# Optimization experiments

Hardware: AMD Instinct MI355X
Metric: run time of the kernel (lower is better)

The kernel has to match this reference:

```python
import jax, jax.numpy as jnp
import numpy as np

B, D, G, L = 8, 128, 2048, 24
GF = G // 2 + 1  # rfft bins
EPS = 1e-5


def setup_inputs() -> dict:
    key = jax.random.key(0)
    ks = jax.random.split(key, 6)
    x = jax.random.normal(ks[0], (B, D, G), dtype=jnp.float32)
    Phi_f = jax.random.normal(ks[1], (L, GF), dtype=jnp.float32) * 0.1
    Theta = jax.random.normal(ks[2], (L, D, D), dtype=jnp.float32) * (1.0 / np.sqrt(D))
    ln_gamma = jnp.ones((D,), dtype=jnp.float32)
    ln_beta = jnp.zeros((D,), dtype=jnp.float32)
    fc1_w = jax.random.normal(ks[3], (2 * D, D), dtype=jnp.float32) * (1.0 / np.sqrt(D))
    fc1_b = jnp.zeros((2 * D,), dtype=jnp.float32)
    fc2_w = jax.random.normal(ks[4], (D, 2 * D), dtype=jnp.float32) * (1.0 / np.sqrt(2 * D))
    fc2_b = jnp.zeros((D,), dtype=jnp.float32)
    return {
        'x': x, 'Phi_f': Phi_f, 'Theta': Theta,
        'ln_gamma': ln_gamma, 'ln_beta': ln_beta,
        'fc1_w': fc1_w, 'fc1_b': fc1_b, 'fc2_w': fc2_w, 'fc2_b': fc2_b,
    }


def reference(x, Phi_f, Theta, ln_gamma, ln_beta, fc1_w, fc1_b, fc2_w, fc2_b):
    # x: (B, D, G). LayerNorm over the lifting (channel) dim D.
    mean = jnp.mean(x, axis=1, keepdims=True)
    var = jnp.var(x, axis=1, keepdims=True)
    z = (x - mean) * jax.lax.rsqrt(var + EPS)
    z = z * ln_gamma[None, :, None] + ln_beta[None, :, None]

    # Spectral convolution with each Hilbert filter.
    Xf = jnp.fft.rfft(z, axis=-1)                       # (B, D, GF) complex
    Uf = Xf[:, :, None, :] * jnp.conj(Phi_f)[None, None]  # (B, D, L, GF)
    U = jnp.fft.irfft(Uf, n=G, axis=-1)                 # (B, D, L, G)

    # Per-filter channel mixing then reduction over filters:
    # einsum('bdln,lhd->bhln') followed by sum over l, fused:
    S = jnp.einsum('bdlg,lhd->bhg', U, Theta)           # (B, D, G)

    # Pointwise MLP (Conv1d kernel_size=1 == channel matmul).
    H = jnp.einsum('hd,bdg->bhg', fc1_w, S) + fc1_b[None, :, None]
    H = jax.nn.gelu(H, approximate=False)
    out = jnp.einsum('dh,bhg->bdg', fc2_w, H) + fc2_b[None, :, None]
    return x + out
```

## Files before the change

### kernel.cpp

```cpp
#include <hip/hip_runtime.h>
#include <math.h>


#define B_   8
#define D_   128
#define G_   2048
#define L_   24
#define GF_  1025
#define BD_  1024
#define C2_  2050
#define CP_  2080
#define MW_  2176
#define KP2_ 2112
#define DD_  16384

#define PB_GWI0 2176
#define PB_LN0  4224
#define PB_CV0  4288
#define PB_TT0  4354
#define PB_END  4610

typedef __attribute__((ext_vector_type(8))) short  short8v;
typedef __attribute__((ext_vector_type(4))) float  float4v;

union FU { float f; unsigned int u; };
union V8 { short8v v; ushort u[8]; };
union V4 { uint2 p; ushort u[4]; };

static __device__ __forceinline__ float bf2f(ushort h) {
    FU v; v.u = ((unsigned int)h) << 16; return v.f;
}
static __device__ __forceinline__ ushort f2bf(float f) {
    FU v; v.f = f;
    unsigned int r = v.u + 0x7fffu + ((v.u >> 16) & 1u);
    return (ushort)(r >> 16);
}
static __device__ __forceinline__ void async16(const void* g, void* l) {
    __builtin_amdgcn_global_load_lds(
        (const __attribute__((address_space(1))) void*)g,
        (__attribute__((address_space(3))) void*)l, 16, 0, 0);
}
static __device__ __forceinline__ int is_f32(const unsigned int* graw) {
    return graw[0] == 0x3F800000u;
}

__global__ __launch_bounds__(256) void k_pre(
        const void* __restrict__ x_raw,  const void* __restrict__ th_raw,
        const unsigned int* __restrict__ graw, const void* __restrict__ be_raw,
        const void* __restrict__ w1_raw, const void* __restrict__ b1_raw,
        const void* __restrict__ w2_raw, const void* __restrict__ b2_raw,
        ushort* __restrict__ z,  ushort* __restrict__ wf,
        ushort* __restrict__ wi, ushort* __restrict__ thT,
        ushort* __restrict__ w1c, ushort* __restrict__ b1c,
        ushort* __restrict__ w2c, ushort* __restrict__ b2c) {
    __shared__ ushort T[L_][72];
    int bid = blockIdx.x, tid = threadIdx.x;

    if (bid < PB_GWI0) {
        int c  = bid;
        int g0 = tid * 8;
        V8 v;
        if (c >= C2_) {
            #pragma unroll
            for (int j = 0; j < 8; ++j) v.u[j] = 0;
        } else {
            int f = c >> 1, im = c & 1;
            #pragma unroll
            for (int j = 0; j < 8; ++j) {
                int g = g0 + j;
                int r = (f * g) & (G_ - 1);
                float th = (float)r * (6.283185307179586f / (float)G_);
                v.u[j] = f2bf(im ? -__sinf(th) : __cosf(th));
            }
        }
        *(short8v*)(wf + (size_t)c * G_ + g0) = v.v;
    } else if (bid < PB_LN0) {
        int g = bid - PB_GWI0;
        for (int ch = tid; ch < KP2_ / 8; ch += 256) {
            int c0 = ch * 8;
            V8 v;
            #pragma unroll
            for (int j = 0; j < 8; ++j) {
                int c = c0 + j;
                if (c >= C2_) { v.u[j] = 0; continue; }
                int f = c >> 1, im = c & 1;
                float a = (f == 0 || f == G_ / 2) ? (1.f / G_) : (2.f / G_);
                int r = (f * g) & (G_ - 1);
                float th = (float)r * (6.283185307179586f / (float)G_);
                v.u[j] = f2bf(im ? -a * __sinf(th) : a * __cosf(th));
            }
            *(short8v*)(wi + (size_t)g * KP2_ + c0) = v.v;
        }
    } else if (bid < PB_CV0) {
        int fl = is_f32(graw);
        int lb = bid - PB_LN0;
        int b  = lb >> 3;
        int g  = (lb & 7) * 256 + tid;
        float s = 0.f, ss = 0.f;
        if (fl) {
            const float* xp = (const float*)x_raw + (size_t)b * D_ * G_ + g;
            for (int d = 0; d < D_; ++d) {
                float v = xp[(size_t)d * G_];
                s += v; ss += v * v;
            }
        } else {
            const ushort* xp = (const ushort*)x_raw + (size_t)b * D_ * G_ + g;
            for (int d = 0; d < D_; ++d) {
                float v = bf2f(xp[(size_t)d * G_]);
                s += v; ss += v * v;
            }
        }
        float mean = s * (1.f / D_);
        float var  = ss * (1.f / D_) - mean * mean;
        float inv  = rsqrtf(var + 1e-5f);
        ushort* zp = z + (size_t)b * D_ * G_ + g;
        if (fl) {
            const float* xp = (const float*)x_raw + (size_t)b * D_ * G_ + g;
            const float* gp = (const float*)graw;
            const float* bp = (const float*)be_raw;
            for (int d = 0; d < D_; ++d) {
                float o = (xp[(size_t)d * G_] - mean) * inv * gp[d] + bp[d];
                zp[(size_t)d * G_] = f2bf(o);
            }
        } else {
            const ushort* xp = (const ushort*)x_raw + (size_t)b * D_ * G_ + g;
            const ushort* gp = (const ushort*)graw;
            const ushort* bp = (const ushort*)be_raw;
            for (int d = 0; d < D_; ++d) {
                float o = (bf2f(xp[(size_t)d * G_]) - mean) * inv * bf2f(gp[d])
                        + bf2f(bp[d]);
                zp[(size_t)d * G_] = f2bf(o);
            }
        }
    } else if (bid < PB_TT0) {
        int fl = is_f32(graw);
        int lb = bid - PB_CV0;
        const void* src; ushort* dst; int n, rel;
        if (lb < 32)       { src = w1_raw; dst = w1c; n = 32768; rel = lb; }
        else if (lb == 32) { src = b1_raw; dst = b1c; n = 256;   rel = 0; }
        else if (lb < 65)  { src = w2_raw; dst = w2c; n = 32768; rel = lb - 33; }
        else               { src = b2_raw; dst = b2c; n = 128;   rel = 0; }
        int i0 = rel * 1024 + tid * 4;
        if (fl) {
            const float* s = (const float*)src;
            #pragma unroll
            for (int j = 0; j < 4; ++j) {
                int k = i0 + j;
                if (k < n) dst[k] = f2bf(s[k]);
            }
        } else {
            const ushort* s = (const ushort*)src;
            #pragma unroll
            for (int j = 0; j < 4; ++j) {
                int k = i0 + j;
                if (k < n) dst[k] = s[k];
            }
        }
    } else {
        int fl = is_f32(graw);
        int hd0 = (bid - PB_TT0) * 64;
        if (tid < 192) {
            int l = tid >> 3, c8 = tid & 7;
            V8 o;
            if (fl) {
                const float* tp = (const float*)th_raw + (size_t)l * DD_ +
                                  hd0 + c8 * 8;
                float4v a0 = *(const float4v*)tp;
                float4v a1 = *(const float4v*)(tp + 4);
                #pragma unroll
                for (int j = 0; j < 4; ++j) {
                    o.u[j] = f2bf(a0[j]); o.u[4 + j] = f2bf(a1[j]);
                }
            } else {
                o.v = *(const short8v*)((const ushort*)th_raw +
                                        (size_t)l * DD_ + hd0 + c8 * 8);
            }
            *(short8v*)&T[l][c8 * 8] = o.v;
        }
        __syncthreads();
        int hdl = tid & 63, part = tid >> 6;
        V8 o;
        #pragma unroll
        for (int j = 0; j < 8; ++j) {
            int l = part * 8 + j;
            o.u[j] = (l < L_) ? T[l][hdl] : (ushort)0;
        }
        *(short8v*)(thT + (size_t)(hd0 + hdl) * 32 + part * 8) = o.v;
    }
}

__global__ __launch_bounds__(256) void k_buildM5(const void* __restrict__ phi_raw,
                                                 const unsigned int* __restrict__ graw,
                                                 const ushort* __restrict__ thT,
                                                 ushort* __restrict__ M) {
    __shared__ ushort Aph[16][40];
    int isf = is_f32(graw);
    int f0  = blockIdx.x * 16;
    int hd0 = blockIdx.y * 256;
    int tid = threadIdx.x;
    #pragma unroll
    for (int rep = 0; rep < 2; ++rep) {
        int idx = rep * 256 + tid;
        int fl = idx >> 5, l = idx & 31;
        int f = f0 + fl;
        ushort v = 0;
        if (l < L_ && f < GF_)
            v = isf ? f2bf(((const float*)phi_raw)[(size_t)l * GF_ + f])
                    : ((const ushort*)phi_raw)[(size_t)l * GF_ + f];
        Aph[fl][l] = v;
    }
    __syncthreads();
    int w = tid >> 6, lane = tid & 63;
    int lr = lane & 15, q = lane >> 4;
    short8v a = *(const short8v*)&Aph[lr][q * 8];
    #pragma unroll
    for (int t = 0; t < 4; ++t) {
        int n = hd0 + (w * 4 + t) * 16 + lr;
        short8v b = *(const short8v*)(thT + (size_t)n * 32 + q * 8);
        float4v c = {0.f, 0.f, 0.f, 0.f};
        c = __builtin_amdgcn_mfma_f32_16x16x32_bf16(a, b, c, 0, 0, 0);
        #pragma unroll
        for (int r = 0; r < 4; ++r) {
            int f = f0 + q * 4 + r;
            if (f < GF_) M[(size_t)f * DD_ + n] = f2bf(c[r]);
        }
    }
}

__global__ __launch_bounds__(256, 4) void k_gemm64(const ushort* __restrict__ A,
                                                   const ushort* __restrict__ Bm,
                                                   float* __restrict__ C,
                                                   int K, int lda, int ldb, int ldc) {
    __shared__ ushort As[2][64 * 64];
    __shared__ ushort Bs[2][64 * 64];
    int tid = threadIdx.x;
    int m0 = blockIdx.x * 64;
    int n0 = blockIdx.y * 64;
    int w = tid >> 6, lane = tid & 63;
    int lr = lane & 15, q = lane >> 4;
    int wm = (w & 1) * 32, wn = (w >> 1) * 32;

    int rl = lane >> 3, c8 = (lane & 7) ^ rl;
    int t0 = w * 2, t1 = w * 2 + 1;
    const ushort* gA0 = A  + (size_t)(m0 + t0 * 8 + rl) * lda + c8 * 8;
    const ushort* gA1 = A  + (size_t)(m0 + t1 * 8 + rl) * lda + c8 * 8;
    const ushort* gB0 = Bm + (size_t)(n0 + t0 * 8 + rl) * ldb + c8 * 8;
    const ushort* gB1 = Bm + (size_t)(n0 + t1 * 8 + rl) * ldb + c8 * 8;

    float4v acc00 = {0.f,0.f,0.f,0.f}, acc01 = {0.f,0.f,0.f,0.f};
    float4v acc10 = {0.f,0.f,0.f,0.f}, acc11 = {0.f,0.f,0.f,0.f};

    async16(gA0, &As[0][t0 * 512]);
    async16(gA1, &As[0][t1 * 512]);
    async16(gB0, &Bs[0][t0 * 512]);
    async16(gB1, &Bs[0][t1 * 512]);
    __syncthreads();

    int buf = 0;
    for (int k0 = 0; k0 < K; k0 += 64) {
        if (k0 + 64 < K) {
            int nb = buf ^ 1;
            async16(gA0 + k0 + 64, &As[nb][t0 * 512]);
            async16(gA1 + k0 + 64, &As[nb][t1 * 512]);
            async16(gB0 + k0 + 64, &Bs[nb][t0 * 512]);
            async16(gB1 + k0 + 64, &Bs[nb][t1 * 512]);
        }
        const ushort* Ab = &As[buf][0];
        const ushort* Bb = &Bs[buf][0];
        #pragma unroll
        for (int s = 0; s < 2; ++s) {
            int cs = s * 4 + q;
            int ra0 = wm + lr, ra1 = wm + 16 + lr;
            int rb0 = wn + lr, rb1 = wn + 16 + lr;
            short8v a0 = *(const short8v*)(Ab + ra0 * 64 + ((cs ^ (ra0 & 7)) << 3));
            short8v a1 = *(const short8v*)(Ab + ra1 * 64 + ((cs ^ (ra1 & 7)) << 3));
            short8v b0 = *(const short8v*)(Bb + rb0 * 64 + ((cs ^ (rb0 & 7)) << 3));
            short8v b1 = *(const short8v*)(Bb + rb1 * 64 + ((cs ^ (rb1 & 7)) << 3));
            acc00 = __builtin_amdgcn_mfma_f32_16x16x32_bf16(a0, b0, acc00, 0, 0, 0);
            acc01 = __builtin_amdgcn_mfma_f32_16x16x32_bf16(a0, b1, acc01, 0, 0, 0);
            acc10 = __builtin_amdgcn_mfma_f32_16x16x32_bf16(a1, b0, acc10, 0, 0, 0);
            acc11 = __builtin_amdgcn_mfma_f32_16x16x32_bf16(a1, b1, acc11, 0, 0, 0);
        }
        __syncthreads();
        buf ^= 1;
    }

    float4v accs[2][2] = { { acc00, acc01 }, { acc10, acc11 } };
    #pragma unroll
    for (int i = 0; i < 2; ++i)
        #pragma unroll
        for (int j = 0; j < 2; ++j) {
            int col = n0 + wn + j * 16 + lr;
            int row = m0 + wm + i * 16 + q * 4;
            #pragma unroll
            for (int r = 0; r < 4; ++r)
                C[(size_t)(row + r) * ldc + col] = accs[i][j][r];
        }
}

__global__ __launch_bounds__(256, 2) void k_mix3(const float* __restrict__ zft,
                                                 const ushort* __restrict__ M,
                                                 ushort* __restrict__ sft) {
    int f   = blockIdx.x;
    int tid = threadIdx.x;
    if (f >= GF_) {
        V8 zv;
        #pragma unroll
        for (int j = 0; j < 8; ++j) zv.u[j] = 0;
        *(short8v*)(sft + (size_t)2 * f * BD_ + tid * 8) = zv.v;
        return;
    }
    int w = tid >> 6, lane = tid & 63;
    int lr = lane & 15, q = lane >> 4;

    int cc = lr >> 3, bb = lr & 7;
    const float* zrow = zft + (size_t)(2 * f + cc) * BD_ + bb * 128 + q * 8;
    short8v a[4];
    #pragma unroll
    for (int s = 0; s < 4; ++s) {
        float4v v0 = *(const float4v*)(zrow + s * 32);
        float4v v1 = *(const float4v*)(zrow + s * 32 + 4);
        V8 t;
        t.u[0] = f2bf(v0[0]); t.u[1] = f2bf(v0[1]);
        t.u[2] = f2bf(v0[2]); t.u[3] = f2bf(v0[3]);
        t.u[4] = f2bf(v1[0]); t.u[5] = f2bf(v1[1]);
        t.u[6] = f2bf(v1[2]); t.u[7] = f2bf(v1[3]);
        a[s] = t.v;
    }

    const ushort* Mf = M + (size_t)f * DD_;
    #pragma unroll
    for (int n = 0; n < 2; ++n) {
        int nt = 2 * w + n;
        float4v c = {0.f, 0.f, 0.f, 0.f};
        #pragma unroll
        for (int s = 0; s < 4; ++s) {
            short8v bfr = *(const short8v*)(Mf + (size_t)(nt * 16 + lr) * D_ +
                                            s * 32 + q * 8);
            c = __builtin_amdgcn_mfma_f32_16x16x32_bf16(a[s], bfr, c, 0, 0, 0);
        }
        #pragma unroll
        for (int r = 0; r < 4; ++r) {
            int p  = q * 4 + r;
            int c2 = p >> 3, b2 = p & 7;
            sft[(size_t)(2 * f + c2) * BD_ + b2 * 128 + nt * 16 + lr] = f2bf(c[r]);
        }
    }
}

__global__ __launch_bounds__(256) void k_tr(const ushort* __restrict__ sft,
                                            ushort* __restrict__ sftT) {
    __shared__ ushort T[64][72];
    int c0 = blockIdx.x * 64, n0 = blockIdx.y * 64;
    int tid = threadIdx.x;
    int r = tid >> 3, c8 = tid & 7;
    #pragma unroll
    for (int h = 0; h < 2; ++h) {
        int cr = c0 + h * 32 + r;
        V8 v;
        if (cr < CP_) {
            v.v = *(const short8v*)(sft + (size_t)cr * BD_ + n0 + c8 * 8);
        } else {
            #pragma unroll
            for (int j = 0; j < 8; ++j) v.u[j] = 0;
        }
        *(short8v*)&T[h * 32 + r][c8 * 8] = v.v;
    }
    __syncthreads();
    #pragma unroll
    for (int h = 0; h < 2; ++h) {
        int rn = h * 32 + r;
        V8 o;
        #pragma unroll
        for (int j = 0; j < 8; ++j) o.u[j] = T[c8 * 8 + j][rn];
        *(short8v*)(sftT + (size_t)(n0 + rn) * KP2_ + c0 + c8 * 8) = o.v;
    }
}

#define MLPG 32
__global__ __launch_bounds__(256, 2) void k_mlp2(const float* __restrict__ ST,
                                                 const void* __restrict__ x0,
                                                 const ushort* __restrict__ w1,
                                                 const ushort* __restrict__ b1,
                                                 const ushort* __restrict__ w2,
                                                 const ushort* __restrict__ b2,
                                                 const unsigned int* __restrict__ graw,
                                                 void* __restrict__ outv) {
    __shared__ ushort Sb[MLPG][136];
    __shared__ ushort Hb[MLPG][264];
    int g0 = blockIdx.x * MLPG, b = blockIdx.y;
    int tid = threadIdx.x;
    {
        int col = tid >> 3, seg = tid & 7;
        const float* sp = ST + (size_t)(g0 + col) * BD_ + b * D_ + seg * 16;
        float4v v0 = *(const float4v*)(sp);
        float4v v1 = *(const float4v*)(sp + 4);
        float4v v2 = *(const float4v*)(sp + 8);
        float4v v3 = *(const float4v*)(sp + 12);
        V8 o0, o1;
        #pragma unroll
        for (int k = 0; k < 4; ++k) { o0.u[k] = f2bf(v0[k]); o0.u[4 + k] = f2bf(v1[k]); }
        #pragma unroll
        for (int k = 0; k < 4; ++k) { o1.u[k] = f2bf(v2[k]); o1.u[4 + k] = f2bf(v3[k]); }
        *(short8v*)&Sb[col][seg * 16]     = o0.v;
        *(short8v*)&Sb[col][seg * 16 + 8] = o1.v;
    }
    __syncthreads();
    int w = tid >> 6, lane = tid & 63;
    int lr = lane & 15, q = lane >> 4;
    int nt = w & 1, mh = w >> 1;

    {
        float4v acc[8];
        #pragma unroll
        for (int i = 0; i < 8; ++i) { float4v zz = {0.f,0.f,0.f,0.f}; acc[i] = zz; }
        #pragma unroll
        for (int ks = 0; ks < 4; ++ks) {
            short8v bf = *(const short8v*)&Sb[nt * 16 + lr][ks * 32 + q * 8];
            #pragma unroll
            for (int i = 0; i < 8; ++i) {
                int mt = mh * 8 + i;
                short8v af = *(const short8v*)(w1 + (size_t)(mt * 16 + lr) * D_ +
                                               ks * 32 + q * 8);
                acc[i] = __builtin_amdgcn_mfma_f32_16x16x32_bf16(af, bf, acc[i], 0, 0, 0);
            }
        }
        #pragma unroll
        for (int i = 0; i < 8; ++i) {
            int h0 = (mh * 8 + i) * 16 + q * 4;
            V4 hv;
            #pragma unroll
            for (int r = 0; r < 4; ++r) {
                float v = acc[i][r] + bf2f(b1[h0 + r]);
                v = 0.5f * v * (1.f + erff(v * 0.70710678118f));
                hv.u[r] = f2bf(v);
            }
            *(uint2*)&Hb[nt * 16 + lr][h0] = hv.p;
        }
    }
    __syncthreads();
    {
        float4v acc2[4];
        #pragma unroll
        for (int j = 0; j < 4; ++j) { float4v zz = {0.f,0.f,0.f,0.f}; acc2[j] = zz; }
        #pragma unroll
        for (int ks = 0; ks < 8; ++ks) {
            short8v bf = *(const short8v*)&Hb[nt * 16 + lr][ks * 32 + q * 8];
            #pragma unroll
            for (int j = 0; j < 4; ++j) {
                int mt2 = mh * 4 + j;
                short8v af = *(const short8v*)(w2 + (size_t)(mt2 * 16 + lr) * (2 * D_) +
                                               ks * 32 + q * 8);
                acc2[j] = __builtin_amdgcn_mfma_f32_16x16x32_bf16(af, bf, acc2[j], 0, 0, 0);
            }
        }
        int col = g0 + nt * 16 + lr;
        int fl = is_f32(graw);
        #pragma unroll
        for (int j = 0; j < 4; ++j) {
            int d0 = (mh * 4 + j) * 16 + q * 4;
            #pragma unroll
            for (int r = 0; r < 4; ++r) {
                int d = d0 + r;
                float v = acc2[j][r] + bf2f(b2[d]);
                size_t idx = ((size_t)(b * D_ + d)) * G_ + col;
                if (fl) {
                    ((float*)outv)[idx] = v + ((const float*)x0)[idx];
                } else {
                    ((ushort*)outv)[idx] =
                        f2bf(v + bf2f(((const ushort*)x0)[idx]));
                }
            }
        }
    }
}

extern "C" void kernel_launch(void* const* d_in, const int* in_sizes, int n_in,
                              void* d_out, int out_size, void* d_ws, size_t ws_size,
                              hipStream_t stream) {
    char* base = (char*)d_ws;
    ushort* z    = (ushort*)(base);
    ushort* wf   = (ushort*)(base + 4194304);
    ushort* sft  = (ushort*)(base);
    ushort* thT  = (ushort*)(base + 13107200);
    float*  zft  = (float*)(base + 13107200);
    float*  st   = (float*)(base + 13107200);
    ushort* w1c  = (ushort*)(base + 27050048);
    ushort* b1c  = (ushort*)(base + 27115584);
    ushort* w2c  = (ushort*)(base + 27116096);
    ushort* b2c  = (ushort*)(base + 27181632);
    ushort* Mm   = (ushort*)(base + 27182592);
    ushort* sftT = (ushort*)(base + 27182592);
    ushort* wi   = (ushort*)(base + 60769792);

    const unsigned int* graw = (const unsigned int*)d_in[3];

    k_pre    <<<dim3(PB_END), 256, 0, stream>>>(
        d_in[0], d_in[2], graw, d_in[4], d_in[5], d_in[6], d_in[7], d_in[8],
        z, wf, wi, thT, w1c, b1c, w2c, b2c);
    k_buildM5<<<dim3(66, DD_ / 256), 256, 0, stream>>>(d_in[1], graw, thT, Mm);
    k_gemm64 <<<dim3(MW_ / 64, BD_ / 64), 256, 0, stream>>>(
        wf, z, zft, G_, G_, G_, BD_);
    k_mix3   <<<dim3(CP_ / 2), 256, 0, stream>>>(zft, Mm, sft);
    k_tr     <<<dim3(KP2_ / 64, BD_ / 64), 256, 0, stream>>>(sft, sftT);
    k_gemm64 <<<dim3(G_ / 64, BD_ / 64), 256, 0, stream>>>(
        wi, sftT, st, KP2_, KP2_, KP2_, BD_);
    k_mlp2   <<<dim3(G_ / MLPG, B_), 256, 0, stream>>>(st, d_in[0], w1c, b1c,
                                                       w2c, b2c, graw, d_out);
}
```

Before: 195.1 us.

## Fuse forward DFT GEMM with filter build and fold transpose into inverse GEMM

Measured after the change: 191.7 us. About the same (-1.8%).

```diff
diff --git a/kernel.cpp b/kernel.cpp
--- a/kernel.cpp
+++ b/kernel.cpp
@@ -14,11 +14,14 @@
 #define KP2_ 2112
 #define DD_  16384
 
-#define PB_GWI0 2176
-#define PB_LN0  4224
-#define PB_CV0  4288
-#define PB_TT0  4354
-#define PB_END  4610
+#define PA_CV0 64
+#define PA_TT0 130
+#define PA_WF0 386
+#define PA_WI0 2562
+#define PA_END 4610
+
+#define G1_NB  544
+#define G1_END 4768
 
 typedef __attribute__((ext_vector_type(8))) short  short8v;
 typedef __attribute__((ext_vector_type(4))) float  float4v;
@@ -56,46 +59,10 @@
     __shared__ ushort T[L_][72];
     int bid = blockIdx.x, tid = threadIdx.x;
 
-    if (bid < PB_GWI0) {
-        int c  = bid;
-        int g0 = tid * 8;
-        V8 v;
-        if (c >= C2_) {
-            #pragma unroll
-            for (int j = 0; j < 8; ++j) v.u[j] = 0;
-        } else {
-            int f = c >> 1, im = c & 1;
-            #pragma unroll
-            for (int j = 0; j < 8; ++j) {
-                int g = g0 + j;
-                int r = (f * g) & (G_ - 1);
-                float th = (float)r * (6.283185307179586f / (float)G_);
-                v.u[j] = f2bf(im ? -__sinf(th) : __cosf(th));
-            }
-        }
-        *(short8v*)(wf + (size_t)c * G_ + g0) = v.v;
-    } else if (bid < PB_LN0) {
-        int g = bid - PB_GWI0;
-        for (int ch = tid; ch < KP2_ / 8; ch += 256) {
-            int c0 = ch * 8;
-            V8 v;
-            #pragma unroll
-            for (int j = 0; j < 8; ++j) {
-                int c = c0 + j;
-                if (c >= C2_) { v.u[j] = 0; continue; }
-                int f = c >> 1, im = c & 1;
-                float a = (f == 0 || f == G_ / 2) ? (1.f / G_) : (2.f / G_);
-                int r = (f * g) & (G_ - 1);
-                float th = (float)r * (6.283185307179586f / (float)G_);
-                v.u[j] = f2bf(im ? -a * __sinf(th) : a * __cosf(th));
-            }
-            *(short8v*)(wi + (size_t)g * KP2_ + c0) = v.v;
-        }
-    } else if (bid < PB_CV0) {
+    if (bid < PA_CV0) {
         int fl = is_f32(graw);
-        int lb = bid - PB_LN0;
-        int b  = lb >> 3;
-        int g  = (lb & 7) * 256 + tid;
+        int b  = bid >> 3;
+        int g  = (bid & 7) * 256 + tid;
         float s = 0.f, ss = 0.f;
         if (fl) {
             const float* xp = (const float*)x_raw + (size_t)b * D_ * G_ + g;
@@ -132,9 +99,9 @@
                 zp[(size_t)d * G_] = f2bf(o);
             }
         }
-    } else if (bid < PB_TT0) {
+    } else if (bid < PA_TT0) {
         int fl = is_f32(graw);
-        int lb = bid - PB_CV0;
+        int lb = bid - PA_CV0;
         const void* src; ushort* dst; int n, rel;
         if (lb < 32)       { src = w1_raw; dst = w1c; n = 32768; rel = lb; }
         else if (lb == 32) { src = b1_raw; dst = b1c; n = 256;   rel = 0; }
@@ -156,9 +123,9 @@
                 if (k < n) dst[k] = s[k];
             }
         }
-    } else {
+    } else if (bid < PA_WF0) {
         int fl = is_f32(graw);
-        int hd0 = (bid - PB_TT0) * 64;
+        int hd0 = (bid - PA_TT0) * 64;
         if (tid < 192) {
             int l = tid >> 3, c8 = tid & 7;
             V8 o;
@@ -186,116 +153,147 @@
             o.u[j] = (l < L_) ? T[l][hdl] : (ushort)0;
         }
         *(short8v*)(thT + (size_t)(hd0 + hdl) * 32 + part * 8) = o.v;
-    }
-}
-
-__global__ __launch_bounds__(256) void k_buildM5(const void* __restrict__ phi_raw,
-                                                 const unsigned int* __restrict__ graw,
-                                                 const ushort* __restrict__ thT,
-                                                 ushort* __restrict__ M) {
+    } else if (bid < PA_WI0) {
+        int c  = bid - PA_WF0;
+        int g0 = tid * 8;
+        V8 v;
+        if (c >= C2_) {
+            #pragma unroll
+            for (int j = 0; j < 8; ++j) v.u[j] = 0;
+        } else {
+            int f = c >> 1, im = c & 1;
+            #pragma unroll
+            for (int j = 0; j < 8; ++j) {
+                int g = g0 + j;
+                int r = (f * g) & (G_ - 1);
+                float th = (float)r * (6.283185307179586f / (float)G_);
+                v.u[j] = f2bf(im ? -__sinf(th) : __cosf(th));
+            }
+        }
+        *(short8v*)(wf + (size_t)c * G_ + g0) = v.v;
+    } else {
+        int g = bid - PA_WI0;
+        for (int ch = tid; ch < KP2_ / 8; ch += 256) {
+            int c0 = ch * 8;
+            V8 v;
+            #pragma unroll
+            for (int j = 0; j < 8; ++j) {
+                int c = c0 + j;
+                if (c >= C2_) { v.u[j] = 0; continue; }
+                int f = c >> 1, im = c & 1;
+                float a = (f == 0 || f == G_ / 2) ? (1.f / G_) : (2.f / G_);
+                int r = (f * g) & (G_ - 1);
+                float th = (float)r * (6.283185307179586f / (float)G_);
+                v.u[j] = f2bf(im ? -a * __sinf(th) : a * __cosf(th));
+            }
+            *(short8v*)(wi + (size_t)g * KP2_ + c0) = v.v;
+        }
+    }
+}
+
+__global__ __launch_bounds__(256, 4) void k_g1(
+        const ushort* __restrict__ wf, const ushort* __restrict__ z,
+        float* __restrict__ zft,
+        const void* __restrict__ phi_raw, const unsigned int* __restrict__ graw,
+        const ushort* __restrict__ thT, ushort* __restrict__ M) {
+    __shared__ ushort As[2][64 * 64];
+    __shared__ ushort Bs[2][64 * 64];
     __shared__ ushort Aph[16][40];
-    int isf = is_f32(graw);
-    int f0  = blockIdx.x * 16;
-    int hd0 = blockIdx.y * 256;
-    int tid = threadIdx.x;
-    #pragma unroll
-    for (int rep = 0; rep < 2; ++rep) {
-        int idx = rep * 256 + tid;
-        int fl = idx >> 5, l = idx & 31;
-        int f = f0 + fl;
-        ushort v = 0;
-        if (l < L_ && f < GF_)
-            v = isf ? f2bf(((const float*)phi_raw)[(size_t)l * GF_ + f])
-                    : ((const ushort*)phi_raw)[(size_t)l * GF_ + f];
-        Aph[fl][l] = v;
-    }
-    __syncthreads();
+    int bid = blockIdx.x, tid = threadIdx.x;
     int w = tid >> 6, lane = tid & 63;
     int lr = lane & 15, q = lane >> 4;
-    short8v a = *(const short8v*)&Aph[lr][q * 8];
-    #pragma unroll
-    for (int t = 0; t < 4; ++t) {
-        int n = hd0 + (w * 4 + t) * 16 + lr;
-        short8v b = *(const short8v*)(thT + (size_t)n * 32 + q * 8);
-        float4v c = {0.f, 0.f, 0.f, 0.f};
-        c = __builtin_amdgcn_mfma_f32_16x16x32_bf16(a, b, c, 0, 0, 0);
-        #pragma unroll
-        for (int r = 0; r < 4; ++r) {
-            int f = f0 + q * 4 + r;
-            if (f < GF_) M[(size_t)f * DD_ + n] = f2bf(c[r]);
-        }
-    }
-}
-
-__global__ __launch_bounds__(256, 4) void k_gemm64(const ushort* __restrict__ A,
-                                                   const ushort* __restrict__ Bm,
-                                                   float* __restrict__ C,
-                                                   int K, int lda, int ldb, int ldc) {
-    __shared__ ushort As[2][64 * 64];
-    __shared__ ushort Bs[2][64 * 64];
-    int tid = threadIdx.x;
-    int m0 = blockIdx.x * 64;
-    int n0 = blockIdx.y * 64;
-    int w = tid >> 6, lane = tid & 63;
-    int lr = lane & 15, q = lane >> 4;
-    int wm = (w & 1) * 32, wn = (w >> 1) * 32;
-
-    int rl = lane >> 3, c8 = (lane & 7) ^ rl;
-    int t0 = w * 2, t1 = w * 2 + 1;
-    const ushort* gA0 = A  + (size_t)(m0 + t0 * 8 + rl) * lda + c8 * 8;
-    const ushort* gA1 = A  + (size_t)(m0 + t1 * 8 + rl) * lda + c8 * 8;
-    const ushort* gB0 = Bm + (size_t)(n0 + t0 * 8 + rl) * ldb + c8 * 8;
-    const ushort* gB1 = Bm + (size_t)(n0 + t1 * 8 + rl) * ldb + c8 * 8;
-
-    float4v acc00 = {0.f,0.f,0.f,0.f}, acc01 = {0.f,0.f,0.f,0.f};
-    float4v acc10 = {0.f,0.f,0.f,0.f}, acc11 = {0.f,0.f,0.f,0.f};
-
-    async16(gA0, &As[0][t0 * 512]);
-    async16(gA1, &As[0][t1 * 512]);
-    async16(gB0, &Bs[0][t0 * 512]);
-    async16(gB1, &Bs[0][t1 * 512]);
-    __syncthreads();
-
-    int buf = 0;
-    for (int k0 = 0; k0 < K; k0 += 64) {
-        if (k0 + 64 < K) {
-            int nb = buf ^ 1;
-            async16(gA0 + k0 + 64, &As[nb][t0 * 512]);
-            async16(gA1 + k0 + 64, &As[nb][t1 * 512]);
-            async16(gB0 + k0 + 64, &Bs[nb][t0 * 512]);
-            async16(gB1 + k0 + 64, &Bs[nb][t1 * 512]);
-        }
-        const ushort* Ab = &As[buf][0];
-        const ushort* Bb = &Bs[buf][0];
-        #pragma unroll
-        for (int s = 0; s < 2; ++s) {
-            int cs = s * 4 + q;
-            int ra0 = wm + lr, ra1 = wm + 16 + lr;
-            int rb0 = wn + lr, rb1 = wn + 16 + lr;
-            short8v a0 = *(const short8v*)(Ab + ra0 * 64 + ((cs ^ (ra0 & 7)) << 3));
-            short8v a1 = *(const short8v*)(Ab + ra1 * 64 + ((cs ^ (ra1 & 7)) << 3));
-            short8v b0 = *(const short8v*)(Bb + rb0 * 64 + ((cs ^ (rb0 & 7)) << 3));
-            short8v b1 = *(const short8v*)(Bb + rb1 * 64 + ((cs ^ (rb1 & 7)) << 3));
-            acc00 = __builtin_amdgcn_mfma_f32_16x16x32_bf16(a0, b0, acc00, 0, 0, 0);
-            acc01 = __builtin_amdgcn_mfma_f32_16x16x32_bf16(a0, b1, acc01, 0, 0, 0);
-            acc10 = __builtin_amdgcn_mfma_f32_16x16x32_bf16(a1, b0, acc10, 0, 0, 0);
-            acc11 = __builtin_amdgcn_mfma_f32_16x16x32_bf16(a1, b1, acc11, 0, 0, 0);
-        }
+
+    if (bid < G1_NB) {
+        int m0 = (bid >> 4) * 64;
+        int n0 = (bid & 15) * 64;
+        int wm = (w & 1) * 32, wn = (w >> 1) * 32;
+        int rl = lane >> 3, c8 = (lane & 7) ^ rl;
+        int t0 = w * 2, t1 = w * 2 + 1;
+        const ushort* gA0 = wf + (size_t)(m0 + t0 * 8 + rl) * G_ + c8 * 8;
+        const ushort* gA1 = wf + (size_t)(m0 + t1 * 8 + rl) * G_ + c8 * 8;
+        const ushort* gB0 = z  + (size_t)(n0 + t0 * 8 + rl) * G_ + c8 * 8;
+        const ushort* gB1 = z  + (size_t)(n0 + t1 * 8 + rl) * G_ + c8 * 8;
+
+        float4v acc00 = {0.f,0.f,0.f,0.f}, acc01 = {0.f,0.f,0.f,0.f};
+        float4v acc10 = {0.f,0.f,0.f,0.f}, acc11 = {0.f,0.f,0.f,0.f};
+
+        async16(gA0, &As[0][t0 * 512]);
+        async16(gA1, &As[0][t1 * 512]);
+        async16(gB0, &Bs[0][t0 * 512]);
+        async16(gB1, &Bs[0][t1 * 512]);
         __syncthreads();
-        buf ^= 1;
-    }
-
-    float4v accs[2][2] = { { acc00, acc01 }, { acc10, acc11 } };
-    #pragma unroll
-    for (int i = 0; i < 2; ++i)
-        #pragma unroll
-        for (int j = 0; j < 2; ++j) {
-            int col = n0 + wn + j * 16 + lr;
-            int row = m0 + wm + i * 16 + q * 4;
-            #pragma unroll
-            for (int r = 0; r < 4; ++r)
-                C[(size_t)(row + r) * ldc + col] = accs[i][j][r];
-        }
+
+        int buf = 0;
+        for (int k0 = 0; k0 < G_; k0 += 64) {
+            if (k0 + 64 < G_) {
+                int nb = buf ^ 1;
+                async16(gA0 + k0 + 64, &As[nb][t0 * 512]);
+                async16(gA1 + k0 + 64, &As[nb][t1 * 512]);
+                async16(gB0 + k0 + 64, &Bs[nb][t0 * 512]);
+                async16(gB1 + k0 + 64, &Bs[nb][t1 * 512]);
+            }
+            const ushort* Ab = &As[buf][0];
+            const ushort* Bb = &Bs[buf][0];
+            #pragma unroll
+            for (int s = 0; s < 2; ++s) {
+                int cs = s * 4 + q;
+                int ra0 = wm + lr, ra1 = wm + 16 + lr;
+                int rb0 = wn + lr, rb1 = wn + 16 + lr;
+                short8v a0 = *(const short8v*)(Ab + ra0 * 64 + ((cs ^ (ra0 & 7)) << 3));
+                short8v a1 = *(const short8v*)(Ab + ra1 * 64 + ((cs ^ (ra1 & 7)) << 3));
+                short8v b0 = *(const short8v*)(Bb + rb0 * 64 + ((cs ^ (rb0 & 7)) << 3));
+                short8v b1 = *(const short8v*)(Bb + rb1 * 64 + ((cs ^ (rb1 & 7)) << 3));
+                acc00 = __builtin_amdgcn_mfma_f32_16x16x32_bf16(a0, b0, acc00, 0, 0, 0);
+                acc01 = __builtin_amdgcn_mfma_f32_16x16x32_bf16(a0, b1, acc01, 0, 0, 0);
+                acc10 = __builtin_amdgcn_mfma_f32_16x16x32_bf16(a1, b0, acc10, 0, 0, 0);
+                acc11 = __builtin_amdgcn_mfma_f32_16x16x32_bf16(a1, b1, acc11, 0, 0, 0);
+            }
+            __syncthreads();
+            buf ^= 1;
+        }
+
+        float4v accs[2][2] = { { acc00, acc01 }, { acc10, acc11 } };
+        #pragma unroll
+        for (int i = 0; i < 2; ++i)
+            #pragma unroll
+            for (int j = 0; j < 2; ++j) {
+                int col = n0 + wn + j * 16 + lr;
+                int row = m0 + wm + i * 16 + q * 4;
+                #pragma unroll
+                for (int r = 0; r < 4; ++r)
+                    zft[(size_t)(row + r) * BD_ + col] = accs[i][j][r];
+            }
+    } else {
+        int bb  = bid - G1_NB;
+        int f0  = (bb >> 6) * 16;
+        int hd0 = (bb & 63) * 256;
+        int isf = is_f32(graw);
+        #pragma unroll
+        for (int rep = 0; rep < 2; ++rep) {
+            int idx = rep * 256 + tid;
+            int fl = idx >> 5, l = idx & 31;
+            int f = f0 + fl;
+            ushort v = 0;
+            if (l < L_ && f < GF_)
+                v = isf ? f2bf(((const float*)phi_raw)[(size_t)l * GF_ + f])
+                        : ((const ushort*)phi_raw)[(size_t)l * GF_ + f];
+            Aph[fl][l] = v;
+        }
+        __syncthreads();
+        short8v a = *(const short8v*)&Aph[lr][q * 8];
+        #pragma unroll
+        for (int t = 0; t < 4; ++t) {
+            int n = hd0 + (w * 4 + t) * 16 + lr;
+            short8v b = *(const short8v*)(thT + (size_t)n * 32 + q * 8);
+            float4v c = {0.f, 0.f, 0.f, 0.f};
+            c = __builtin_amdgcn_mfma_f32_16x16x32_bf16(a, b, c, 0, 0, 0);
+            #pragma unroll
+            for (int r = 0; r < 4; ++r) {
+                int f = f0 + q * 4 + r;
+                if (f < GF_) M[(size_t)f * DD_ + n] = f2bf(c[r]);
+            }
+        }
+    }
 }
 
 __global__ __launch_bounds__(256, 2) void k_mix3(const float* __restrict__ zft,
@@ -303,13 +301,6 @@
                                                  ushort* __restrict__ sft) {
     int f   = blockIdx.x;
     int tid = threadIdx.x;
-    if (f >= GF_) {
-        V8 zv;
-        #pragma unroll
-        for (int j = 0; j < 8; ++j) zv.u[j] = 0;
-        *(short8v*)(sft + (size_t)2 * f * BD_ + tid * 8) = zv.v;
-        return;
-    }
     int w = tid >> 6, lane = tid & 63;
     int lr = lane & 15, q = lane >> 4;
 
@@ -348,33 +339,119 @@
     }
 }
 
-__global__ __launch_bounds__(256) void k_tr(const ushort* __restrict__ sft,
-                                            ushort* __restrict__ sftT) {
-    __shared__ ushort T[64][72];
-    int c0 = blockIdx.x * 64, n0 = blockIdx.y * 64;
+__global__ __launch_bounds__(256, 4) void k_gemm64t(const ushort* __restrict__ A,
+                                                    const ushort* __restrict__ Bm,
+                                                    float* __restrict__ C,
+                                                    int K, int lda, int ldb, int ldc) {
+    __shared__ ushort As[2][64 * 64];
+    __shared__ ushort Bs[2][64 * 64];
     int tid = threadIdx.x;
-    int r = tid >> 3, c8 = tid & 7;
+    int m0 = blockIdx.x * 64, n0 = blockIdx.y * 64;
+    int w = tid >> 6, lane = tid & 63;
+    int lr = lane & 15, q = lane >> 4;
+    int wm = (w & 1) * 32, wn = (w >> 1) * 32;
+
+    int rl = lane >> 3, c8 = (lane & 7) ^ rl;
+    int t0 = w * 2, t1 = w * 2 + 1;
+    const ushort* gA0 = A + (size_t)(m0 + t0 * 8 + rl) * lda + c8 * 8;
+    const ushort* gA1 = A + (size_t)(m0 + t1 * 8 + rl) * lda + c8 * 8;
+
+    int br = tid >> 2;
+    int bc = tid & 3;
+
+    float4v acc00 = {0.f,0.f,0.f,0.f}, acc01 = {0.f,0.f,0.f,0.f};
+    float4v acc10 = {0.f,0.f,0.f,0.f}, acc11 = {0.f,0.f,0.f,0.f};
+
+    async16(gA0, &As[0][t0 * 512]);
+    async16(gA1, &As[0][t1 * 512]);
+    {
+        V8 u0, u1;
+        if (br < C2_) {
+            const ushort* gb = Bm + (size_t)br * ldb + n0 + bc * 16;
+            u0.v = *(const short8v*)gb;
+            u1.v = *(const short8v*)(gb + 8);
+        } else {
+            #pragma unroll
+            for (int j = 0; j < 8; ++j) { u0.u[j] = 0; u1.u[j] = 0; }
+        }
+        int swz = (((br >> 3)) << 3) | (br & 7);
+        #pragma unroll
+        for (int j = 0; j < 8; ++j) {
+            int n = bc * 16 + j;
+            Bs[0][n * 64 + ((((br >> 3) ^ (n & 7)) << 3) | (br & 7))] = u0.u[j];
+        }
+        #pragma unroll
+        for (int j = 0; j < 8; ++j) {
+            int n = bc * 16 + 8 + j;
+            Bs[0][n * 64 + ((((br >> 3) ^ (n & 7)) << 3) | (br & 7))] = u1.u[j];
+        }
+        (void)swz;
+    }
+    __syncthreads();
+
+    int buf = 0;
+    for (int k0 = 0; k0 < K; k0 += 64) {
+        V8 u0, u1;
+        bool more = (k0 + 64 < K);
+        if (more) {
+            int nb = buf ^ 1;
+            async16(gA0 + k0 + 64, &As[nb][t0 * 512]);
+            async16(gA1 + k0 + 64, &As[nb][t1 * 512]);
+            int kr = k0 + 64 + br;
+            if (kr < C2_) {
+                const ushort* gb = Bm + (size_t)kr * ldb + n0 + bc * 16;
+                u0.v = *(const short8v*)gb;
+                u1.v = *(const short8v*)(gb + 8);
+            } else {
+                #pragma unroll
+                for (int j = 0; j < 8; ++j) { u0.u[j] = 0; u1.u[j] = 0; }
+            }
+        }
+        const ushort* Ab = &As[buf][0];
+        const ushort* Bb = &Bs[buf][0];
+        #pragma unroll
+        for (int s = 0; s < 2; ++s) {
+            int cs = s * 4 + q;
+            int ra0 = wm + lr, ra1 = wm + 16 + lr;
+            int rb0 = wn + lr, rb1 = wn + 16 + lr;
+            short8v a0 = *(const short8v*)(Ab + ra0 * 64 + ((cs ^ (ra0 & 7)) << 3));
+            short8v a1 = *(const short8v*)(Ab + ra1 * 64 + ((cs ^ (ra1 & 7)) << 3));
+            short8v b0 = *(const short8v*)(Bb + rb0 * 64 + ((cs ^ (rb0 & 7)) << 3));
+            short8v b1 = *(const short8v*)(Bb + rb1 * 64 + ((cs ^ (rb1 & 7)) << 3));
+            acc00 = __builtin_amdgcn_mfma_f32_16x16x32_bf16(a0, b0, acc00, 0, 0, 0);
+            acc01 = __builtin_amdgcn_mfma_f32_16x16x32_bf16(a0, b1, acc01, 0, 0, 0);
+            acc10 = __builtin_amdgcn_mfma_f32_16x16x32_bf16(a1, b0, acc10, 0, 0, 0);
+            acc11 = __builtin_amdgcn_mfma_f32_16x16x32_bf16(a1, b1, acc11, 0, 0, 0);
+        }
+        __syncthreads();
+        if (more) {
+            int nb = buf ^ 1;
+            #pragma unroll
+            for (int j = 0; j < 8; ++j) {
+                int n = bc * 16 + j;
+                Bs[nb][n * 64 + ((((br >> 3) ^ (n & 7)) << 3) | (br & 7))] = u0.u[j];
+            }
+            #pragma unroll
+            for (int j = 0; j < 8; ++j) {
+                int n = bc * 16 + 8 + j;
+                Bs[nb][n * 64 + ((((br >> 3) ^ (n & 7)) << 3) | (br & 7))] = u1.u[j];
+            }
+        }
+        __syncthreads();
+        buf ^= 1;
+    }
+
+    float4v accs[2][2] = { { acc00, acc01 }, { acc10, acc11 } };
     #pragma unroll
-    for (int h = 0; h < 2; ++h) {
-        int cr = c0 + h * 32 + r;
-        V8 v;
-        if (cr < CP_) {
-            v.v = *(const short8v*)(sft + (size_t)cr * BD_ + n0 + c8 * 8);
-        } else {
-            #pragma unroll
-            for (int j = 0; j < 8; ++j) v.u[j] = 0;
-        }
-        *(short8v*)&T[h * 32 + r][c8 * 8] = v.v;
-    }
-    __syncthreads();
-    #pragma unroll
-    for (int h = 0; h < 2; ++h) {
-        int rn = h * 32 + r;
-        V8 o;
-        #pragma unroll
-        for (int j = 0; j < 8; ++j) o.u[j] = T[c8 * 8 + j][rn];
-        *(short8v*)(sftT + (size_t)(n0 + rn) * KP2_ + c0 + c8 * 8) = o.v;
-    }
+    for (int i = 0; i < 2; ++i)
+        #pragma unroll
+        for (int j = 0; j < 2; ++j) {
+            int col = n0 + wn + j * 16 + lr;
+            int row = m0 + wm + i * 16 + q * 4;
+            #pragma unroll
+            for (int r = 0; r < 4; ++r)
+                C[(size_t)(row + r) * ldc + col] = accs[i][j][r];
+        }
 }
 
 #define MLPG 32
@@ -482,7 +559,6 @@
     ushort* z    = (ushort*)(base);
     ushort* wf   = (ushort*)(base + 4194304);
     ushort* sft  = (ushort*)(base);
-    ushort* thT  = (ushort*)(base + 13107200);
     float*  zft  = (float*)(base + 13107200);
     float*  st   = (float*)(base + 13107200);
     ushort* w1c  = (ushort*)(base + 27050048);
@@ -490,21 +566,19 @@
     ushort* w2c  = (ushort*)(base + 27116096);
     ushort* b2c  = (ushort*)(base + 27181632);
     ushort* Mm   = (ushort*)(base + 27182592);
-    ushort* sftT = (ushort*)(base + 27182592);
     ushort* wi   = (ushort*)(base + 60769792);
+    ushort* thT  = (ushort*)(base + 69420544);
 
     const unsigned int* graw = (const unsigned int*)d_in[3];
 
-    k_pre    <<<dim3(PB_END), 256, 0, stream>>>(
+    k_pre    <<<dim3(PA_END), 256, 0, stream>>>(
         d_in[0], d_in[2], graw, d_in[4], d_in[5], d_in[6], d_in[7], d_in[8],
         z, wf, wi, thT, w1c, b1c, w2c, b2c);
-    k_buildM5<<<dim3(66, DD_ / 256), 256, 0, stream>>>(d_in[1], graw, thT, Mm);
-    k_gemm64 <<<dim3(MW_ / 64, BD_ / 64), 256, 0, stream>>>(
-        wf, z, zft, G_, G_, G_, BD_);
-    k_mix3   <<<dim3(CP_ / 2), 256, 0, stream>>>(zft, Mm, sft);
-    k_tr     <<<dim3(KP2_ / 64, BD_ / 64), 256, 0, stream>>>(sft, sftT);
-    k_gemm64 <<<dim3(G_ / 64, BD_ / 64), 256, 0, stream>>>(
-        wi, sftT, st, KP2_, KP2_, KP2_, BD_);
+    k_g1     <<<dim3(G1_END), 256, 0, stream>>>(wf, z, zft, d_in[1], graw,
+                                                thT, Mm);
+    k_mix3   <<<dim3(GF_), 256, 0, stream>>>(zft, Mm, sft);
+    k_gemm64t<<<dim3(G_ / 64, BD_ / 64), 256, 0, stream>>>(
+        wi, sft, st, KP2_, KP2_, BD_, BD_);
     k_mlp2   <<<dim3(G_ / MLPG, B_), 256, 0, stream>>>(st, d_in[0], w1c, b1c,
                                                        w2c, b2c, graw, d_out);
 }
```
